# Performance work log

Hardware: AMD Instinct MI355X
Metric: run time of the kernel (lower is better)

The kernel has to match this reference:

```python
import jax, jax.numpy as jnp
import numpy as np

# (dv=3, dc=6)-regular Tanner graph: M checks, N=2M vars, E=M*dc edges
M, N, DV, DC, D, B, T = 1024, 2048, 3, 6, 8, 128, 5
CIN = DC * D          # check-MLP in/out dim = 48
VIN = DV * D + 1      # var-MLP in/out dim  = 25 (extra scalar = LLR)
HC, HV = 4 * CIN, 4 * VIN
EPS = 1e-6


def _graph():
    # variable j connects to checks (j + l) % M, l = 0..DV-1 -> every check has degree DC
    var_nbrs = (np.arange(N)[:, None] + np.arange(DV)[None, :]) % M   # [N, DV] check ids
    # var-edge id e = j*DV + l ; sort edges by check to get check-slot ordering
    order = np.argsort(var_nbrs.reshape(-1), kind='stable')           # check-edge p -> var-edge e
    chk_nbrs = (order // DV).reshape(M, DC)                           # var id in each check slot
    inv_order = np.argsort(order)                                     # var-edge e -> check-edge p
    return chk_nbrs, order, inv_order


def setup_inputs() -> dict:
    key = jax.random.key(0)
    ks = jax.random.split(key, 12)
    chk_nbrs, order, inv_order = _graph()
    prior = np.clip(np.random.default_rng(0).uniform(0.005, 0.05, size=N), EPS, 1 - EPS)
    prior_llr = jnp.asarray(np.log((1.0 - prior) / prior), jnp.float32)

    def lin_w(k, g, nin, nout):
        return jax.random.normal(k, (g, nin, nout), jnp.float32) / np.sqrt(nin)

    def lin_b(k, g, nout):
        return 0.02 * jax.random.normal(k, (g, nout), jnp.float32)

    return {
        "syndromes": jax.random.randint(ks[0], (B, M), 0, 2, jnp.int32),
        "prior_llr": prior_llr,
        "chk_w1": lin_w(ks[1], M, CIN, HC), "chk_b1": lin_b(ks[2], M, HC),
        "chk_w2": lin_w(ks[3], M, HC, CIN), "chk_b2": lin_b(ks[4], M, CIN),
        "var_w1": lin_w(ks[5], N, VIN, HV), "var_b1": lin_b(ks[6], N, HV),
        "var_w2": lin_w(ks[7], N, HV, VIN), "var_b2": lin_b(ks[8], N, VIN),
        "chk_nbrs": jnp.asarray(chk_nbrs, jnp.int32),      # [M, DC] var id per check slot
        "c2v_gather": jnp.asarray(inv_order, jnp.int32),   # var-edge -> check-edge perm
        "v2c_gather": jnp.asarray(order, jnp.int32),       # check-edge -> var-edge perm
    }


def reference(syndromes, prior_llr, chk_w1, chk_b1, chk_w2, chk_b2,
              var_w1, var_b1, var_w2, var_b2, chk_nbrs, c2v_gather, v2c_gather):
    synd_sgn = (1 - 2 * syndromes).astype(jnp.float32)                    # [B, M]
    prior_b = jnp.broadcast_to(prior_llr, (B, N))[..., None]              # [B, N, 1]

    def chk_mlp(x):  # x: [B, M, CIN], per-check grouped GEMM
        h = jax.nn.gelu(jnp.einsum('bmi,mih->bmh', x, chk_w1) + chk_b1, approximate=False)
        return jnp.einsum('bmh,mho->bmo', h, chk_w2) + chk_b2

    def var_mlp(x):  # x: [B, N, VIN]
        h = jax.nn.gelu(jnp.einsum('bni,nih->bnh', x, var_w1) + var_b1, approximate=False)
        return jnp.einsum('bnh,nho->bno', h, var_w2) + var_b2

    # init check in-messages: zeros with first component = prior LLR of neighbor var
    chk_in = jnp.zeros((B, M, DC, D), jnp.float32).at[..., 0].set(prior_llr[chk_nbrs][None])

    def step(chk_in, _):
        y = chk_mlp(chk_in.reshape(B, M, CIN)).reshape(B, M, DC, D)
        y = y * synd_sgn[:, :, None, None]                                # syndrome sign flip
        var_in = y.reshape(B, M * DC, D)[:, c2v_gather]                   # scatter c->v as gather
        x = jnp.concatenate([var_in.reshape(B, N, DV * D), prior_b], axis=-1)
        out = var_mlp(x)
        llr = out[..., DV * D]                                            # [B, N]
        msg = out[..., :DV * D].reshape(B, N * DV, D)
        chk_in_new = msg[:, v2c_gather].reshape(B, M, DC, D)              # scatter v->c as gather
        return chk_in_new, llr

    _, llrs = jax.lax.scan(step, chk_in, None, length=T)
    return llrs  # [T, B, N]
```

## Files before the change

kernel.cpp:

```cpp
#include <hip/hip_runtime.h>
#include <math.h>

#define MM 1024
#define NN 2048
#define BB 128
#define TT 5
#define EE 6144

typedef __bf16 bf16x8 __attribute__((ext_vector_type(8)));
typedef float  f32x4  __attribute__((ext_vector_type(4)));
typedef unsigned int u32x4 __attribute__((ext_vector_type(4)));
typedef unsigned int u32x2 __attribute__((ext_vector_type(2)));

__device__ __forceinline__ float gelu_fast(float x) {
    float xe = x * 0.70710678118654752f;
    float ax = fabsf(xe);
    float t  = __builtin_amdgcn_rcpf(1.0f + 0.3275911f * ax);
    float p  = t * (0.254829592f + t * (-0.284496736f + t * (1.421413741f +
               t * (-1.453152027f + t * 1.061405429f))));
    float er = 1.0f - p * __expf(-xe * xe);
    er = copysignf(er, xe);
    return 0.5f * x * (1.0f + er);
}

__device__ __forceinline__ void wave_lds_fence() {
    asm volatile("s_waitcnt lgkmcnt(0)" ::: "memory");
}

__global__ __launch_bounds__(256)
void init_kernel(const float* __restrict__ prior, __bf16* __restrict__ v2c)
{
    int idx = blockIdx.x * 256 + threadIdx.x;
    int e = idx >> 7;
    bf16x8 v;
    #pragma unroll
    for (int j = 0; j < 8; ++j) v[j] = (__bf16)0.0f;
    v[0] = (__bf16)prior[e / 3];
    *(bf16x8*)(v2c + (size_t)idx * 8) = v;
}

__global__ __launch_bounds__(256)
void prep_all(const float* __restrict__ cw1, const float* __restrict__ cw2,
              const float* __restrict__ vw1, const float* __restrict__ vw2,
              __bf16* __restrict__ wchk, __bf16* __restrict__ wvar)
{
    const int wid = blockIdx.x * 4 + (threadIdx.x >> 6);
    const int l = threadIdx.x & 63, qq = l >> 4, cc = l & 15;
    bf16x8 v;
    __bf16* dst;
    if (wid < MM * 42) {
        const int m = wid / 42, f = wid % 42;
        if (f < 24) {
            const int kt = f / 12, nt = f % 12;
            const float* s1 = cw1 + (size_t)m * (48 * 192);
            #pragma unroll
            for (int j = 0; j < 8; ++j) {
                int k = kt * 32 + qq * 8 + j;
                v[j] = (k < 48) ? (__bf16)s1[k * 192 + nt * 16 + cc] : (__bf16)0.0f;
            }
        } else {
            const int g = f - 24, kt = g / 3, nt = g % 3;
            const float* s2 = cw2 + (size_t)m * (192 * 48);
            #pragma unroll
            for (int j = 0; j < 8; ++j) {
                int k = kt * 32 + qq * 8 + j;
                v[j] = (__bf16)s2[k * 48 + nt * 16 + cc];
            }
        }
        dst = wchk + (size_t)m * 21504 + (f * 64 + l) * 8;
    } else {
        const int tsk = wid - MM * 42;
        const int nv = tsk / 15, f = tsk % 15;
        if (f < 7) {
            const float* s1 = vw1 + (size_t)nv * (25 * 100);
            #pragma unroll
            for (int j = 0; j < 8; ++j) {
                int k = qq * 8 + j, n = f * 16 + cc;
                v[j] = (k < 25 && n < 100) ? (__bf16)s1[k * 100 + n] : (__bf16)0.0f;
            }
        } else {
            const int g = f - 7, kt = g >> 1, nt = g & 1;
            const float* s2 = vw2 + (size_t)nv * (100 * 25);
            #pragma unroll
            for (int j = 0; j < 8; ++j) {
                int k = kt * 32 + qq * 8 + j, n = nt * 16 + cc;
                v[j] = (k < 100 && n < 25) ? (__bf16)s2[k * 25 + n] : (__bf16)0.0f;
            }
        }
        dst = wvar + (size_t)nv * 7680 + (f * 64 + l) * 8;
    }
    *(bf16x8*)dst = v;
}

__global__ __launch_bounds__(256, 4)
void chk_kernel(const __bf16* __restrict__ wchk,
                const float* __restrict__ b1g, const float* __restrict__ b2g,
                const int* __restrict__ syndromes,
                const int* __restrict__ v2c_gather,
                const __bf16* __restrict__ v2c, __bf16* __restrict__ c2v)
{
    const int m = blockIdx.x;
    const int tid = threadIdx.x;
    const int w = tid >> 6, l = tid & 63, q = l >> 4, c = l & 15;

    __shared__ __align__(16) __bf16 hb[4 * 3200];
    __bf16* myh = hb + w * 3200;

    const __bf16* wb = wchk + (size_t)m * 21504;

    float b1v[12], b2v[3], sg[8];
    #pragma unroll
    for (int nt = 0; nt < 12; ++nt) b1v[nt] = b1g[(size_t)m * 192 + nt * 16 + c];
    #pragma unroll
    for (int nt = 0; nt < 3; ++nt)  b2v[nt] = b2g[(size_t)m * 48 + nt * 16 + c];
    #pragma unroll
    for (int t2 = 0; t2 < 2; ++t2)
        #pragma unroll
        for (int r = 0; r < 4; ++r) {
            int row = t2 * 64 + w * 16 + q * 4 + r;
            sg[t2 * 4 + r] = (float)(1 - 2 * syndromes[(size_t)row * MM + m]);
        }

    const int e0 = v2c_gather[m * 6 + q];
    const int e1 = (q < 2) ? v2c_gather[m * 6 + 4 + q] : 0;

    for (int t2 = 0; t2 < 2; ++t2) {
        const int bt = t2 * 64 + w * 16;

        bf16x8 a0 = *(const bf16x8*)(v2c + ((size_t)e0 * BB + bt + c) * 8);
        bf16x8 a1;
        #pragma unroll
        for (int j = 0; j < 8; ++j) a1[j] = (__bf16)0.0f;
        if (q < 2) a1 = *(const bf16x8*)(v2c + ((size_t)e1 * BB + bt + c) * 8);

        f32x4 acc[12];
        #pragma unroll
        for (int nt = 0; nt < 12; ++nt) {
            bf16x8 bf0 = *(const bf16x8*)(wb + (nt * 64 + l) * 8);
            bf16x8 bf1 = *(const bf16x8*)(wb + ((12 + nt) * 64 + l) * 8);
            f32x4 z = {0.f, 0.f, 0.f, 0.f};
            z = __builtin_amdgcn_mfma_f32_16x16x32_bf16(a0, bf0, z, 0, 0, 0);
            z = __builtin_amdgcn_mfma_f32_16x16x32_bf16(a1, bf1, z, 0, 0, 0);
            acc[nt] = z;
        }

        #pragma unroll
        for (int nt = 0; nt < 12; ++nt) {
            #pragma unroll
            for (int r = 0; r < 4; ++r) {
                int row = q * 4 + r;
                myh[row * 200 + nt * 16 + c] = (__bf16)gelu_fast(acc[nt][r] + b1v[nt]);
            }
        }
        wave_lds_fence();

        f32x4 acc2[3];
        #pragma unroll
        for (int nt = 0; nt < 3; ++nt) acc2[nt] = (f32x4){0.f, 0.f, 0.f, 0.f};
        #pragma unroll
        for (int kt = 0; kt < 6; ++kt) {
            bf16x8 a = *(const bf16x8*)(myh + c * 200 + kt * 32 + q * 8);
            #pragma unroll
            for (int nt = 0; nt < 3; ++nt) {
                bf16x8 bfr = *(const bf16x8*)(wb + ((24 + kt * 3 + nt) * 64 + l) * 8);
                acc2[nt] = __builtin_amdgcn_mfma_f32_16x16x32_bf16(a, bfr, acc2[nt], 0, 0, 0);
            }
        }
        wave_lds_fence();

        #pragma unroll
        for (int nt = 0; nt < 3; ++nt) {
            #pragma unroll
            for (int r = 0; r < 4; ++r) {
                int row = q * 4 + r;
                myh[row * 72 + nt * 16 + c] = (__bf16)((acc2[nt][r] + b2v[nt]) * sg[t2 * 4 + r]);
            }
        }
        wave_lds_fence();

        {
            int s = l >> 4, row = l & 15;
            u32x4 vv = *(const u32x4*)(myh + row * 72 + s * 8);
            *(u32x4*)(c2v + ((size_t)(m * 6 + s) * BB + bt + row) * 8) = vv;
            if (l < 32) {
                int s2 = 4 + (l >> 4), row2 = l & 15;
                u32x4 v2 = *(const u32x4*)(myh + row2 * 72 + s2 * 8);
                *(u32x4*)(c2v + ((size_t)(m * 6 + s2) * BB + bt + row2) * 8) = v2;
            }
        }
        wave_lds_fence();
    }
}

__global__ __launch_bounds__(256, 4)
void var_kernel(const __bf16* __restrict__ wvar,
                const float* __restrict__ b1g, const float* __restrict__ b2g,
                const int* __restrict__ c2v_gather, const float* __restrict__ prior,
                const __bf16* __restrict__ c2v, __bf16* __restrict__ v2c,
                float* __restrict__ llr_out, int last)
{
    const int nv = blockIdx.x;
    const int tid = threadIdx.x;
    const int w = tid >> 6, l = tid & 63, q = l >> 4, c = l & 15;

    __shared__ __align__(16) __bf16 hb[4 * 2816];
    __bf16* myh = hb + w * 2816;
    __bf16* myy = myh + 2176;

    const __bf16* wb = wvar + (size_t)nv * 7680;

    {
        int r = l >> 2, g = l & 3;
        *(u32x2*)(myh + r * 136 + 112 + g * 4) = (u32x2){0, 0};
    }

    float b1v[7], b2v[2];
    #pragma unroll
    for (int nt = 0; nt < 7; ++nt) {
        int col = nt * 16 + c;
        b1v[nt] = (col < 100) ? b1g[(size_t)nv * 100 + col] : 0.0f;
    }
    #pragma unroll
    for (int nt = 0; nt < 2; ++nt) {
        int col = nt * 16 + c;
        b2v[nt] = (col < 25) ? b2g[(size_t)nv * 25 + col] : 0.0f;
    }
    const __bf16 prbf = (__bf16)prior[nv];
    const int ep = (q < 3) ? c2v_gather[nv * 3 + q] : 0;

    for (int t2 = 0; t2 < 2; ++t2) {
        const int bt = t2 * 64 + w * 16;

        bf16x8 a;
        #pragma unroll
        for (int j = 0; j < 8; ++j) a[j] = (__bf16)0.0f;
        if (q < 3) a = *(const bf16x8*)(c2v + ((size_t)ep * BB + bt + c) * 8);
        else       a[0] = prbf;

        f32x4 acc[7];
        #pragma unroll
        for (int nt = 0; nt < 7; ++nt) {
            bf16x8 bfr = *(const bf16x8*)(wb + (nt * 64 + l) * 8);
            f32x4 z = {0.f, 0.f, 0.f, 0.f};
            acc[nt] = __builtin_amdgcn_mfma_f32_16x16x32_bf16(a, bfr, z, 0, 0, 0);
        }

        #pragma unroll
        for (int nt = 0; nt < 7; ++nt) {
            #pragma unroll
            for (int r = 0; r < 4; ++r) {
                int row = q * 4 + r;
                myh[row * 136 + nt * 16 + c] = (__bf16)gelu_fast(acc[nt][r] + b1v[nt]);
            }
        }
        wave_lds_fence();

        f32x4 acc2[2];
        acc2[0] = (f32x4){0.f, 0.f, 0.f, 0.f};
        acc2[1] = (f32x4){0.f, 0.f, 0.f, 0.f};
        #pragma unroll
        for (int kt = 0; kt < 4; ++kt) {
            bf16x8 a2 = *(const bf16x8*)(myh + c * 136 + kt * 32 + q * 8);
            #pragma unroll
            for (int nt = 0; nt < 2; ++nt) {
                bf16x8 bfr = *(const bf16x8*)(wb + ((7 + kt * 2 + nt) * 64 + l) * 8);
                acc2[nt] = __builtin_amdgcn_mfma_f32_16x16x32_bf16(a2, bfr, acc2[nt], 0, 0, 0);
            }
        }
        wave_lds_fence();

        #pragma unroll
        for (int nt = 0; nt < 2; ++nt) {
            #pragma unroll
            for (int r = 0; r < 4; ++r) {
                int row = q * 4 + r, col = nt * 16 + c;
                float yv = acc2[nt][r] + b2v[nt];
                if (col < 24) myy[row * 40 + col] = (__bf16)yv;
                else if (col == 24) llr_out[(size_t)(bt + row) * NN + nv] = yv;
            }
        }
        wave_lds_fence();

        if (!last && l < 48) {
            int s = l >> 4, row = l & 15;
            u32x4 vv = *(const u32x4*)(myy + row * 40 + s * 8);
            *(u32x4*)(v2c + ((size_t)(nv * 3 + s) * BB + bt + row) * 8) = vv;
        }
        wave_lds_fence();
    }
}

extern "C" void kernel_launch(void* const* d_in, const int* in_sizes, int n_in,
                              void* d_out, int out_size, void* d_ws, size_t ws_size,
                              hipStream_t stream) {
    const int*   syndromes = (const int*)  d_in[0];
    const float* prior_llr = (const float*)d_in[1];
    const float* chk_w1    = (const float*)d_in[2];
    const float* chk_b1    = (const float*)d_in[3];
    const float* chk_w2    = (const float*)d_in[4];
    const float* chk_b2    = (const float*)d_in[5];
    const float* var_w1    = (const float*)d_in[6];
    const float* var_b1    = (const float*)d_in[7];
    const float* var_w2    = (const float*)d_in[8];
    const float* var_b2    = (const float*)d_in[9];
    const int*   c2v_g     = (const int*)  d_in[11];
    const int*   v2c_g     = (const int*)  d_in[12];

    float* out = (float*)d_out;

    __bf16* v2c  = (__bf16*)d_ws;
    __bf16* c2v  = v2c + (size_t)EE * BB * 8;
    __bf16* wchk = c2v + (size_t)EE * BB * 8;
    __bf16* wvar = wchk + (size_t)MM * 21504;

    prep_all<<<(MM * 42 + NN * 15) / 4, 256, 0, stream>>>(chk_w1, chk_w2,
                                                          var_w1, var_w2,
                                                          wchk, wvar);
    init_kernel<<<EE * BB / 256, 256, 0, stream>>>(prior_llr, v2c);

    for (int t = 0; t < TT; ++t) {
        chk_kernel<<<MM, 256, 0, stream>>>(wchk, chk_b1, chk_b2,
                                           syndromes, v2c_g, v2c, c2v);
        var_kernel<<<NN, 256, 0, stream>>>(wvar, var_b1, var_b2,
                                           c2v_g, prior_llr, c2v, v2c,
                                           out + (size_t)t * BB * NN,
                                           (t == TT - 1) ? 1 : 0);
    }
}
```

Before: 443.8 us.

## Stage per-node MLP weights in LDS and chunk check hidden layer

The check and variable kernels now copy each node's pre-packed bf16 weights into shared memory once per block, instead of having every wave read them from global memory on each batch half. The check kernel splits the hidden layer into three chunks of 64 columns that are fused into the second GEMM, which shrinks per-wave scratch space and register use. The prep kernel is reworked to issue unconditional clamped loads before masking, and the check kernel's occupancy hint drops to three blocks per CU to fit the larger LDS footprint. The trade-offs are an extra block-wide barrier plus lower occupancy, set against fewer redundant global and L2 weight reads.

```diff
diff --git a/kernel.cpp b/kernel.cpp
--- a/kernel.cpp
+++ b/kernel.cpp
@@ -46,6 +46,7 @@
 {
     const int wid = blockIdx.x * 4 + (threadIdx.x >> 6);
     const int l = threadIdx.x & 63, qq = l >> 4, cc = l & 15;
+    float tmp[8];
     bf16x8 v;
     __bf16* dst;
     if (wid < MM * 42) {
@@ -56,16 +57,21 @@
             #pragma unroll
             for (int j = 0; j < 8; ++j) {
                 int k = kt * 32 + qq * 8 + j;
-                v[j] = (k < 48) ? (__bf16)s1[k * 192 + nt * 16 + cc] : (__bf16)0.0f;
+                tmp[j] = s1[min(k, 47) * 192 + nt * 16 + cc];
+            }
+            #pragma unroll
+            for (int j = 0; j < 8; ++j) {
+                int k = kt * 32 + qq * 8 + j;
+                v[j] = (k < 48) ? (__bf16)tmp[j] : (__bf16)0.0f;
             }
         } else {
             const int g = f - 24, kt = g / 3, nt = g % 3;
             const float* s2 = cw2 + (size_t)m * (192 * 48);
             #pragma unroll
-            for (int j = 0; j < 8; ++j) {
-                int k = kt * 32 + qq * 8 + j;
-                v[j] = (__bf16)s2[k * 48 + nt * 16 + cc];
-            }
+            for (int j = 0; j < 8; ++j)
+                tmp[j] = s2[(kt * 32 + qq * 8 + j) * 48 + nt * 16 + cc];
+            #pragma unroll
+            for (int j = 0; j < 8; ++j) v[j] = (__bf16)tmp[j];
         }
         dst = wchk + (size_t)m * 21504 + (f * 64 + l) * 8;
     } else {
@@ -73,18 +79,30 @@
         const int nv = tsk / 15, f = tsk % 15;
         if (f < 7) {
             const float* s1 = vw1 + (size_t)nv * (25 * 100);
-            #pragma unroll
-            for (int j = 0; j < 8; ++j) {
-                int k = qq * 8 + j, n = f * 16 + cc;
-                v[j] = (k < 25 && n < 100) ? (__bf16)s1[k * 100 + n] : (__bf16)0.0f;
+            const int n = f * 16 + cc, nc = min(n, 99);
+            #pragma unroll
+            for (int j = 0; j < 8; ++j) {
+                int k = qq * 8 + j;
+                tmp[j] = s1[min(k, 24) * 100 + nc];
+            }
+            #pragma unroll
+            for (int j = 0; j < 8; ++j) {
+                int k = qq * 8 + j;
+                v[j] = (k < 25 && n < 100) ? (__bf16)tmp[j] : (__bf16)0.0f;
             }
         } else {
             const int g = f - 7, kt = g >> 1, nt = g & 1;
             const float* s2 = vw2 + (size_t)nv * (100 * 25);
-            #pragma unroll
-            for (int j = 0; j < 8; ++j) {
-                int k = kt * 32 + qq * 8 + j, n = nt * 16 + cc;
-                v[j] = (k < 100 && n < 25) ? (__bf16)s2[k * 25 + n] : (__bf16)0.0f;
+            const int n = nt * 16 + cc, nc = min(n, 24);
+            #pragma unroll
+            for (int j = 0; j < 8; ++j) {
+                int k = kt * 32 + qq * 8 + j;
+                tmp[j] = s2[min(k, 99) * 25 + nc];
+            }
+            #pragma unroll
+            for (int j = 0; j < 8; ++j) {
+                int k = kt * 32 + qq * 8 + j;
+                v[j] = (k < 100 && n < 25) ? (__bf16)tmp[j] : (__bf16)0.0f;
             }
         }
         dst = wvar + (size_t)nv * 7680 + (f * 64 + l) * 8;
@@ -92,7 +110,7 @@
     *(bf16x8*)dst = v;
 }
 
-__global__ __launch_bounds__(256, 4)
+__global__ __launch_bounds__(256, 3)
 void chk_kernel(const __bf16* __restrict__ wchk,
                 const float* __restrict__ b1g, const float* __restrict__ b2g,
                 const int* __restrict__ syndromes,
@@ -103,10 +121,14 @@
     const int tid = threadIdx.x;
     const int w = tid >> 6, l = tid & 63, q = l >> 4, c = l & 15;
 
-    __shared__ __align__(16) __bf16 hb[4 * 3200];
-    __bf16* myh = hb + w * 3200;
-
-    const __bf16* wb = wchk + (size_t)m * 21504;
+    __shared__ __align__(16) __bf16 wlds[21504];
+    __shared__ __align__(16) __bf16 scr[4 * 1152];
+
+    {
+        const __bf16* src = wchk + (size_t)m * 21504;
+        for (int i = tid; i < 2688; i += 256)
+            *(u32x4*)(wlds + i * 8) = *(const u32x4*)(src + i * 8);
+    }
 
     float b1v[12], b2v[3], sg[8];
     #pragma unroll
@@ -120,10 +142,13 @@
             int row = t2 * 64 + w * 16 + q * 4 + r;
             sg[t2 * 4 + r] = (float)(1 - 2 * syndromes[(size_t)row * MM + m]);
         }
-
     const int e0 = v2c_gather[m * 6 + q];
     const int e1 = (q < 2) ? v2c_gather[m * 6 + 4 + q] : 0;
 
+    __syncthreads();
+
+    __bf16* myc = scr + w * 1152;
+
     for (int t2 = 0; t2 < 2; ++t2) {
         const int bt = t2 * 64 + w * 16;
 
@@ -133,58 +158,64 @@
         for (int j = 0; j < 8; ++j) a1[j] = (__bf16)0.0f;
         if (q < 2) a1 = *(const bf16x8*)(v2c + ((size_t)e1 * BB + bt + c) * 8);
 
-        f32x4 acc[12];
-        #pragma unroll
-        for (int nt = 0; nt < 12; ++nt) {
-            bf16x8 bf0 = *(const bf16x8*)(wb + (nt * 64 + l) * 8);
-            bf16x8 bf1 = *(const bf16x8*)(wb + ((12 + nt) * 64 + l) * 8);
-            f32x4 z = {0.f, 0.f, 0.f, 0.f};
-            z = __builtin_amdgcn_mfma_f32_16x16x32_bf16(a0, bf0, z, 0, 0, 0);
-            z = __builtin_amdgcn_mfma_f32_16x16x32_bf16(a1, bf1, z, 0, 0, 0);
-            acc[nt] = z;
-        }
-
-        #pragma unroll
-        for (int nt = 0; nt < 12; ++nt) {
+        f32x4 acc2[3];
+        #pragma unroll
+        for (int nt = 0; nt < 3; ++nt) acc2[nt] = (f32x4){0.f, 0.f, 0.f, 0.f};
+
+        #pragma unroll
+        for (int ch = 0; ch < 3; ++ch) {
+            f32x4 acc[4];
+            #pragma unroll
+            for (int lnt = 0; lnt < 4; ++lnt) {
+                int nt = ch * 4 + lnt;
+                bf16x8 bf0 = *(const bf16x8*)(wlds + (nt * 64 + l) * 8);
+                bf16x8 bf1 = *(const bf16x8*)(wlds + ((12 + nt) * 64 + l) * 8);
+                f32x4 z = {0.f, 0.f, 0.f, 0.f};
+                z = __builtin_amdgcn_mfma_f32_16x16x32_bf16(a0, bf0, z, 0, 0, 0);
+                z = __builtin_amdgcn_mfma_f32_16x16x32_bf16(a1, bf1, z, 0, 0, 0);
+                acc[lnt] = z;
+            }
+            #pragma unroll
+            for (int lnt = 0; lnt < 4; ++lnt) {
+                #pragma unroll
+                for (int r = 0; r < 4; ++r) {
+                    int row = q * 4 + r;
+                    myc[row * 72 + lnt * 16 + c] =
+                        (__bf16)gelu_fast(acc[lnt][r] + b1v[ch * 4 + lnt]);
+                }
+            }
+            wave_lds_fence();
+            #pragma unroll
+            for (int ktl = 0; ktl < 2; ++ktl) {
+                bf16x8 aF = *(const bf16x8*)(myc + c * 72 + ktl * 32 + q * 8);
+                #pragma unroll
+                for (int nt = 0; nt < 3; ++nt) {
+                    bf16x8 bfr = *(const bf16x8*)(wlds +
+                        ((24 + (ch * 2 + ktl) * 3 + nt) * 64 + l) * 8);
+                    acc2[nt] = __builtin_amdgcn_mfma_f32_16x16x32_bf16(aF, bfr, acc2[nt], 0, 0, 0);
+                }
+            }
+            wave_lds_fence();
+        }
+
+        #pragma unroll
+        for (int nt = 0; nt < 3; ++nt) {
             #pragma unroll
             for (int r = 0; r < 4; ++r) {
                 int row = q * 4 + r;
-                myh[row * 200 + nt * 16 + c] = (__bf16)gelu_fast(acc[nt][r] + b1v[nt]);
-            }
-        }
-        wave_lds_fence();
-
-        f32x4 acc2[3];
-        #pragma unroll
-        for (int nt = 0; nt < 3; ++nt) acc2[nt] = (f32x4){0.f, 0.f, 0.f, 0.f};
-        #pragma unroll
-        for (int kt = 0; kt < 6; ++kt) {
-            bf16x8 a = *(const bf16x8*)(myh + c * 200 + kt * 32 + q * 8);
-            #pragma unroll
-            for (int nt = 0; nt < 3; ++nt) {
-                bf16x8 bfr = *(const bf16x8*)(wb + ((24 + kt * 3 + nt) * 64 + l) * 8);
-                acc2[nt] = __builtin_amdgcn_mfma_f32_16x16x32_bf16(a, bfr, acc2[nt], 0, 0, 0);
-            }
-        }
-        wave_lds_fence();
-
-        #pragma unroll
-        for (int nt = 0; nt < 3; ++nt) {
-            #pragma unroll
-            for (int r = 0; r < 4; ++r) {
-                int row = q * 4 + r;
-                myh[row * 72 + nt * 16 + c] = (__bf16)((acc2[nt][r] + b2v[nt]) * sg[t2 * 4 + r]);
+                myc[row * 56 + nt * 16 + c] =
+                    (__bf16)((acc2[nt][r] + b2v[nt]) * sg[t2 * 4 + r]);
             }
         }
         wave_lds_fence();
 
         {
             int s = l >> 4, row = l & 15;
-            u32x4 vv = *(const u32x4*)(myh + row * 72 + s * 8);
+            u32x4 vv = *(const u32x4*)(myc + row * 56 + s * 8);
             *(u32x4*)(c2v + ((size_t)(m * 6 + s) * BB + bt + row) * 8) = vv;
             if (l < 32) {
                 int s2 = 4 + (l >> 4), row2 = l & 15;
-                u32x4 v2 = *(const u32x4*)(myh + row2 * 72 + s2 * 8);
+                u32x4 v2 = *(const u32x4*)(myc + row2 * 56 + s2 * 8);
                 *(u32x4*)(c2v + ((size_t)(m * 6 + s2) * BB + bt + row2) * 8) = v2;
             }
         }
@@ -203,11 +234,17 @@
     const int tid = threadIdx.x;
     const int w = tid >> 6, l = tid & 63, q = l >> 4, c = l & 15;
 
+    __shared__ __align__(16) __bf16 wlds[7680];
     __shared__ __align__(16) __bf16 hb[4 * 2816];
+
+    {
+        const __bf16* src = wvar + (size_t)nv * 7680;
+        for (int i = tid; i < 960; i += 256)
+            *(u32x4*)(wlds + i * 8) = *(const u32x4*)(src + i * 8);
+    }
+
     __bf16* myh = hb + w * 2816;
     __bf16* myy = myh + 2176;
-
-    const __bf16* wb = wvar + (size_t)nv * 7680;
 
     {
         int r = l >> 2, g = l & 3;
@@ -228,6 +265,8 @@
     const __bf16 prbf = (__bf16)prior[nv];
     const int ep = (q < 3) ? c2v_gather[nv * 3 + q] : 0;
 
+    __syncthreads();
+
     for (int t2 = 0; t2 < 2; ++t2) {
         const int bt = t2 * 64 + w * 16;
 
@@ -240,7 +279,7 @@
         f32x4 acc[7];
         #pragma unroll
         for (int nt = 0; nt < 7; ++nt) {
-            bf16x8 bfr = *(const bf16x8*)(wb + (nt * 64 + l) * 8);
+            bf16x8 bfr = *(const bf16x8*)(wlds + (nt * 64 + l) * 8);
             f32x4 z = {0.f, 0.f, 0.f, 0.f};
             acc[nt] = __builtin_amdgcn_mfma_f32_16x16x32_bf16(a, bfr, z, 0, 0, 0);
         }
@@ -263,7 +302,7 @@
             bf16x8 a2 = *(const bf16x8*)(myh + c * 136 + kt * 32 + q * 8);
             #pragma unroll
             for (int nt = 0; nt < 2; ++nt) {
-                bf16x8 bfr = *(const bf16x8*)(wb + ((7 + kt * 2 + nt) * 64 + l) * 8);
+                bf16x8 bfr = *(const bf16x8*)(wlds + ((7 + kt * 2 + nt) * 64 + l) * 8);
                 acc2[nt] = __builtin_amdgcn_mfma_f32_16x16x32_bf16(a2, bfr, acc2[nt], 0, 0, 0);
             }
         }
```

After: 416.3 us. 6.2% less time.

## Use transposed MFMA layout, fold biases into weights, stage weights in LDS

Applied to the files above, without the earlier changes.

The MLPs are recomputed in transposed form (weights as the A operand, activations as B). The first layer's output fragments then feed the second layer's 16x16x16 MFMA directly from registers, which removes the LDS round-trip and wave fences for the hidden activations. Biases are folded into the weight matrices through an extra constant-one input row. Per-block weights are copied cooperatively into LDS, and outputs are packed and written straight to global memory. The cost is one block-wide sync per block, more LDS per block (chk occupancy hint lowered to 3), and a slightly larger prepacked weight buffer.

```diff
diff --git a/kernel.cpp b/kernel.cpp
--- a/kernel.cpp
+++ b/kernel.cpp
@@ -8,9 +8,16 @@
 #define EE 6144
 
 typedef __bf16 bf16x8 __attribute__((ext_vector_type(8)));
+typedef __bf16 bf16x4 __attribute__((ext_vector_type(4)));
+typedef short  s16x4  __attribute__((ext_vector_type(4)));
 typedef float  f32x4  __attribute__((ext_vector_type(4)));
 typedef unsigned int u32x4 __attribute__((ext_vector_type(4)));
 typedef unsigned int u32x2 __attribute__((ext_vector_type(2)));
+
+#define CHK_W_ELEMS 22272
+#define CHK_L2_OFF  12288
+#define VAR_W_ELEMS 7168
+#define VAR_L2_OFF  3584
 
 __device__ __forceinline__ float gelu_fast(float x) {
     float xe = x * 0.70710678118654752f;
@@ -23,8 +30,22 @@
     return 0.5f * x * (1.0f + er);
 }
 
-__device__ __forceinline__ void wave_lds_fence() {
-    asm volatile("s_waitcnt lgkmcnt(0)" ::: "memory");
+__device__ __forceinline__ f32x4 mfma16(bf16x4 a, bf16x4 b, f32x4 c) {
+#if __has_builtin(__builtin_amdgcn_mfma_f32_16x16x16bf16_1k)
+    return __builtin_amdgcn_mfma_f32_16x16x16bf16_1k(
+        __builtin_bit_cast(s16x4, a), __builtin_bit_cast(s16x4, b), c, 0, 0, 0);
+#else
+    f32x4 d;
+    asm volatile("v_mfma_f32_16x16x16_bf16 %0, %1, %2, %3\n\ts_nop 4"
+                 : "=v"(d) : "v"(a), "v"(b), "v"(c));
+    return d;
+#endif
+}
+
+__device__ __forceinline__ unsigned pack2(float a, float b) {
+    unsigned short ua = __builtin_bit_cast(unsigned short, (__bf16)a);
+    unsigned short ub = __builtin_bit_cast(unsigned short, (__bf16)b);
+    return (unsigned)ua | ((unsigned)ub << 16);
 }
 
 __global__ __launch_bounds__(256)
@@ -40,61 +61,109 @@
 }
 
 __global__ __launch_bounds__(256)
-void prep_all(const float* __restrict__ cw1, const float* __restrict__ cw2,
-              const float* __restrict__ vw1, const float* __restrict__ vw2,
+void prep_all(const float* __restrict__ cw1, const float* __restrict__ cb1,
+              const float* __restrict__ cw2, const float* __restrict__ cb2,
+              const float* __restrict__ vw1, const float* __restrict__ vb1,
+              const float* __restrict__ vw2, const float* __restrict__ vb2,
               __bf16* __restrict__ wchk, __bf16* __restrict__ wvar)
 {
     const int wid = blockIdx.x * 4 + (threadIdx.x >> 6);
-    const int l = threadIdx.x & 63, qq = l >> 4, cc = l & 15;
-    bf16x8 v;
-    __bf16* dst;
-    if (wid < MM * 42) {
-        const int m = wid / 42, f = wid % 42;
-        if (f < 24) {
-            const int kt = f / 12, nt = f % 12;
-            const float* s1 = cw1 + (size_t)m * (48 * 192);
-            #pragma unroll
-            for (int j = 0; j < 8; ++j) {
-                int k = kt * 32 + qq * 8 + j;
-                v[j] = (k < 48) ? (__bf16)s1[k * 192 + nt * 16 + cc] : (__bf16)0.0f;
+    const int l = threadIdx.x & 63, q = l >> 4, c = l & 15;
+
+    if (wid < 24576) {
+        const int m = wid / 24, f = wid % 24;
+        const int mt = f >> 1, kt = f & 1;
+        const int h = mt * 16 + c;
+        const float* s1 = cw1 + (size_t)m * (48 * 192);
+        float tmp[8];
+        #pragma unroll
+        for (int j = 0; j < 8; ++j) {
+            int k = kt * 32 + q * 8 + j;
+            tmp[j] = s1[min(k, 47) * 192 + h];
+        }
+        float bv = cb1[(size_t)m * 192 + h];
+        bf16x8 v;
+        #pragma unroll
+        for (int j = 0; j < 8; ++j) {
+            int k = kt * 32 + q * 8 + j;
+            float x = (k < 48) ? tmp[j] : ((k == 48) ? bv : 0.0f);
+            v[j] = (__bf16)x;
+        }
+        *(bf16x8*)(wchk + (size_t)m * CHK_W_ELEMS + f * 512 + l * 8) = v;
+    } else if (wid < 37888) {
+        const int t = wid - 24576;
+        const int m = t / 13, ks = t % 13;
+        __bf16* base = wchk + (size_t)m * CHK_W_ELEMS + CHK_L2_OFF;
+        if (ks < 12) {
+            const float* s2 = cw2 + (size_t)m * (192 * 48);
+            #pragma unroll
+            for (int mt = 0; mt < 3; ++mt) {
+                const int o = mt * 16 + c;
+                bf16x4 v;
+                #pragma unroll
+                for (int i = 0; i < 4; ++i)
+                    v[i] = (__bf16)s2[(ks * 16 + q * 4 + i) * 48 + o];
+                *(bf16x4*)(base + (ks * 3 + mt) * 256 + l * 4) = v;
             }
         } else {
-            const int g = f - 24, kt = g / 3, nt = g % 3;
-            const float* s2 = cw2 + (size_t)m * (192 * 48);
-            #pragma unroll
-            for (int j = 0; j < 8; ++j) {
-                int k = kt * 32 + qq * 8 + j;
-                v[j] = (__bf16)s2[k * 48 + nt * 16 + cc];
-            }
-        }
-        dst = wchk + (size_t)m * 21504 + (f * 64 + l) * 8;
+            #pragma unroll
+            for (int mt = 0; mt < 3; ++mt) {
+                const int o = mt * 16 + c;
+                float bv = cb2[(size_t)m * 48 + o];
+                bf16x4 v;
+                #pragma unroll
+                for (int i = 0; i < 4; ++i) v[i] = (__bf16)0.0f;
+                if (q == 0) v[0] = (__bf16)bv;
+                *(bf16x4*)(base + (12 * 3 + mt) * 256 + l * 4) = v;
+            }
+        }
+    } else if (wid < 52224) {
+        const int t = wid - 37888;
+        const int nv = t / 7, mt = t % 7;
+        const int h = mt * 16 + c, hc = min(h, 99);
+        const float* s1 = vw1 + (size_t)nv * (25 * 100);
+        float tmp[8];
+        #pragma unroll
+        for (int j = 0; j < 8; ++j)
+            tmp[j] = s1[min(q * 8 + j, 24) * 100 + hc];
+        float bv = vb1[(size_t)nv * 100 + hc];
+        bf16x8 v;
+        #pragma unroll
+        for (int j = 0; j < 8; ++j) {
+            int k = q * 8 + j;
+            float x = 0.0f;
+            if (h < 100) x = (k < 25) ? tmp[j] : ((k == 25) ? bv : 0.0f);
+            v[j] = (__bf16)x;
+        }
+        *(bf16x8*)(wvar + (size_t)nv * VAR_W_ELEMS + mt * 512 + l * 8) = v;
     } else {
-        const int tsk = wid - MM * 42;
-        const int nv = tsk / 15, f = tsk % 15;
-        if (f < 7) {
-            const float* s1 = vw1 + (size_t)nv * (25 * 100);
-            #pragma unroll
-            for (int j = 0; j < 8; ++j) {
-                int k = qq * 8 + j, n = f * 16 + cc;
-                v[j] = (k < 25 && n < 100) ? (__bf16)s1[k * 100 + n] : (__bf16)0.0f;
-            }
-        } else {
-            const int g = f - 7, kt = g >> 1, nt = g & 1;
-            const float* s2 = vw2 + (size_t)nv * (100 * 25);
-            #pragma unroll
-            for (int j = 0; j < 8; ++j) {
-                int k = kt * 32 + qq * 8 + j, n = nt * 16 + cc;
-                v[j] = (k < 100 && n < 25) ? (__bf16)s2[k * 25 + n] : (__bf16)0.0f;
-            }
-        }
-        dst = wvar + (size_t)nv * 7680 + (f * 64 + l) * 8;
-    }
-    *(bf16x8*)dst = v;
-}
-
-__global__ __launch_bounds__(256, 4)
+        const int t = wid - 52224;
+        const int nv = t / 7, ks = t % 7;
+        const float* s2 = vw2 + (size_t)nv * (100 * 25);
+        __bf16* base = wvar + (size_t)nv * VAR_W_ELEMS + VAR_L2_OFF;
+        #pragma unroll
+        for (int mt = 0; mt < 2; ++mt) {
+            const int o = mt * 16 + c, oc = min(o, 24);
+            float tmp[4];
+            #pragma unroll
+            for (int i = 0; i < 4; ++i)
+                tmp[i] = s2[min(ks * 16 + q * 4 + i, 99) * 25 + oc];
+            float bv = vb2[(size_t)nv * 25 + oc];
+            bf16x4 v;
+            #pragma unroll
+            for (int i = 0; i < 4; ++i) {
+                int k = ks * 16 + q * 4 + i;
+                float x = 0.0f;
+                if (o < 25) x = (k < 100) ? tmp[i] : ((k == 100) ? bv : 0.0f);
+                v[i] = (__bf16)x;
+            }
+            *(bf16x4*)(base + (ks * 2 + mt) * 256 + l * 4) = v;
+        }
+    }
+}
+
+__global__ __launch_bounds__(256, 3)
 void chk_kernel(const __bf16* __restrict__ wchk,
-                const float* __restrict__ b1g, const float* __restrict__ b2g,
                 const int* __restrict__ syndromes,
                 const int* __restrict__ v2c_gather,
                 const __bf16* __restrict__ v2c, __bf16* __restrict__ c2v)
@@ -103,98 +172,71 @@
     const int tid = threadIdx.x;
     const int w = tid >> 6, l = tid & 63, q = l >> 4, c = l & 15;
 
-    __shared__ __align__(16) __bf16 hb[4 * 3200];
-    __bf16* myh = hb + w * 3200;
-
-    const __bf16* wb = wchk + (size_t)m * 21504;
-
-    float b1v[12], b2v[3], sg[8];
-    #pragma unroll
-    for (int nt = 0; nt < 12; ++nt) b1v[nt] = b1g[(size_t)m * 192 + nt * 16 + c];
-    #pragma unroll
-    for (int nt = 0; nt < 3; ++nt)  b2v[nt] = b2g[(size_t)m * 48 + nt * 16 + c];
-    #pragma unroll
-    for (int t2 = 0; t2 < 2; ++t2)
-        #pragma unroll
-        for (int r = 0; r < 4; ++r) {
-            int row = t2 * 64 + w * 16 + q * 4 + r;
-            sg[t2 * 4 + r] = (float)(1 - 2 * syndromes[(size_t)row * MM + m]);
-        }
-
+    __shared__ __align__(16) __bf16 wlds[CHK_W_ELEMS];
+    {
+        const __bf16* src = wchk + (size_t)m * CHK_W_ELEMS;
+        for (int i = tid; i < CHK_W_ELEMS / 8; i += 256)
+            *(u32x4*)(wlds + i * 8) = *(const u32x4*)(src + i * 8);
+    }
     const int e0 = v2c_gather[m * 6 + q];
     const int e1 = (q < 2) ? v2c_gather[m * 6 + 4 + q] : 0;
+    __syncthreads();
 
     for (int t2 = 0; t2 < 2; ++t2) {
         const int bt = t2 * 64 + w * 16;
 
-        bf16x8 a0 = *(const bf16x8*)(v2c + ((size_t)e0 * BB + bt + c) * 8);
-        bf16x8 a1;
-        #pragma unroll
-        for (int j = 0; j < 8; ++j) a1[j] = (__bf16)0.0f;
-        if (q < 2) a1 = *(const bf16x8*)(v2c + ((size_t)e1 * BB + bt + c) * 8);
+        bf16x8 b0 = *(const bf16x8*)(v2c + ((size_t)e0 * BB + bt + c) * 8);
+        bf16x8 b1f;
+        #pragma unroll
+        for (int j = 0; j < 8; ++j) b1f[j] = (__bf16)0.0f;
+        if (q < 2)       b1f = *(const bf16x8*)(v2c + ((size_t)e1 * BB + bt + c) * 8);
+        else if (q == 2) b1f[0] = (__bf16)1.0f;
 
         f32x4 acc[12];
         #pragma unroll
-        for (int nt = 0; nt < 12; ++nt) {
-            bf16x8 bf0 = *(const bf16x8*)(wb + (nt * 64 + l) * 8);
-            bf16x8 bf1 = *(const bf16x8*)(wb + ((12 + nt) * 64 + l) * 8);
+        for (int mt = 0; mt < 12; ++mt) {
+            bf16x8 a0 = *(const bf16x8*)(wlds + (mt * 2 + 0) * 512 + l * 8);
+            bf16x8 a1 = *(const bf16x8*)(wlds + (mt * 2 + 1) * 512 + l * 8);
             f32x4 z = {0.f, 0.f, 0.f, 0.f};
-            z = __builtin_amdgcn_mfma_f32_16x16x32_bf16(a0, bf0, z, 0, 0, 0);
-            z = __builtin_amdgcn_mfma_f32_16x16x32_bf16(a1, bf1, z, 0, 0, 0);
-            acc[nt] = z;
-        }
-
-        #pragma unroll
-        for (int nt = 0; nt < 12; ++nt) {
-            #pragma unroll
-            for (int r = 0; r < 4; ++r) {
-                int row = q * 4 + r;
-                myh[row * 200 + nt * 16 + c] = (__bf16)gelu_fast(acc[nt][r] + b1v[nt]);
-            }
-        }
-        wave_lds_fence();
+            z = __builtin_amdgcn_mfma_f32_16x16x32_bf16(a0, b0, z, 0, 0, 0);
+            z = __builtin_amdgcn_mfma_f32_16x16x32_bf16(a1, b1f, z, 0, 0, 0);
+            acc[mt] = z;
+        }
 
         f32x4 acc2[3];
         #pragma unroll
-        for (int nt = 0; nt < 3; ++nt) acc2[nt] = (f32x4){0.f, 0.f, 0.f, 0.f};
-        #pragma unroll
-        for (int kt = 0; kt < 6; ++kt) {
-            bf16x8 a = *(const bf16x8*)(myh + c * 200 + kt * 32 + q * 8);
-            #pragma unroll
-            for (int nt = 0; nt < 3; ++nt) {
-                bf16x8 bfr = *(const bf16x8*)(wb + ((24 + kt * 3 + nt) * 64 + l) * 8);
-                acc2[nt] = __builtin_amdgcn_mfma_f32_16x16x32_bf16(a, bfr, acc2[nt], 0, 0, 0);
-            }
-        }
-        wave_lds_fence();
-
-        #pragma unroll
-        for (int nt = 0; nt < 3; ++nt) {
-            #pragma unroll
-            for (int r = 0; r < 4; ++r) {
-                int row = q * 4 + r;
-                myh[row * 72 + nt * 16 + c] = (__bf16)((acc2[nt][r] + b2v[nt]) * sg[t2 * 4 + r]);
-            }
-        }
-        wave_lds_fence();
-
-        {
-            int s = l >> 4, row = l & 15;
-            u32x4 vv = *(const u32x4*)(myh + row * 72 + s * 8);
-            *(u32x4*)(c2v + ((size_t)(m * 6 + s) * BB + bt + row) * 8) = vv;
-            if (l < 32) {
-                int s2 = 4 + (l >> 4), row2 = l & 15;
-                u32x4 v2 = *(const u32x4*)(myh + row2 * 72 + s2 * 8);
-                *(u32x4*)(c2v + ((size_t)(m * 6 + s2) * BB + bt + row2) * 8) = v2;
-            }
-        }
-        wave_lds_fence();
+        for (int mt = 0; mt < 3; ++mt) acc2[mt] = (f32x4){0.f, 0.f, 0.f, 0.f};
+        #pragma unroll
+        for (int ks = 0; ks < 13; ++ks) {
+            bf16x4 bf;
+            if (ks < 12) {
+                #pragma unroll
+                for (int r = 0; r < 4; ++r) bf[r] = (__bf16)gelu_fast(acc[ks][r]);
+            } else {
+                #pragma unroll
+                for (int r = 0; r < 4; ++r) bf[r] = (__bf16)0.0f;
+                if (q == 0) bf[0] = (__bf16)1.0f;
+            }
+            #pragma unroll
+            for (int mt = 0; mt < 3; ++mt) {
+                bf16x4 af = *(const bf16x4*)(wlds + CHK_L2_OFF + (ks * 3 + mt) * 256 + l * 4);
+                acc2[mt] = mfma16(af, bf, acc2[mt]);
+            }
+        }
+
+        const float sg = (float)(1 - 2 * syndromes[(size_t)(bt + c) * MM + m]);
+        #pragma unroll
+        for (int mt = 0; mt < 3; ++mt) {
+            u32x2 pv = { pack2(acc2[mt][0] * sg, acc2[mt][1] * sg),
+                         pack2(acc2[mt][2] * sg, acc2[mt][3] * sg) };
+            int s = 2 * mt + (q >> 1);
+            *(u32x2*)(c2v + ((size_t)(m * 6 + s) * BB + bt + c) * 8 + (q & 1) * 4) = pv;
+        }
     }
 }
 
 __global__ __launch_bounds__(256, 4)
 void var_kernel(const __bf16* __restrict__ wvar,
-                const float* __restrict__ b1g, const float* __restrict__ b2g,
                 const int* __restrict__ c2v_gather, const float* __restrict__ prior,
                 const __bf16* __restrict__ c2v, __bf16* __restrict__ v2c,
                 float* __restrict__ llr_out, int last)
@@ -203,90 +245,59 @@
     const int tid = threadIdx.x;
     const int w = tid >> 6, l = tid & 63, q = l >> 4, c = l & 15;
 
-    __shared__ __align__(16) __bf16 hb[4 * 2816];
-    __bf16* myh = hb + w * 2816;
-    __bf16* myy = myh + 2176;
-
-    const __bf16* wb = wvar + (size_t)nv * 7680;
-
+    __shared__ __align__(16) __bf16 wlds[VAR_W_ELEMS];
     {
-        int r = l >> 2, g = l & 3;
-        *(u32x2*)(myh + r * 136 + 112 + g * 4) = (u32x2){0, 0};
-    }
-
-    float b1v[7], b2v[2];
-    #pragma unroll
-    for (int nt = 0; nt < 7; ++nt) {
-        int col = nt * 16 + c;
-        b1v[nt] = (col < 100) ? b1g[(size_t)nv * 100 + col] : 0.0f;
-    }
-    #pragma unroll
-    for (int nt = 0; nt < 2; ++nt) {
-        int col = nt * 16 + c;
-        b2v[nt] = (col < 25) ? b2g[(size_t)nv * 25 + col] : 0.0f;
-    }
+        const __bf16* src = wvar + (size_t)nv * VAR_W_ELEMS;
+        for (int i = tid; i < VAR_W_ELEMS / 8; i += 256)
+            *(u32x4*)(wlds + i * 8) = *(const u32x4*)(src + i * 8);
+    }
+    const int ep = (q < 3) ? c2v_gather[nv * 3 + q] : 0;
     const __bf16 prbf = (__bf16)prior[nv];
-    const int ep = (q < 3) ? c2v_gather[nv * 3 + q] : 0;
+    __syncthreads();
 
     for (int t2 = 0; t2 < 2; ++t2) {
         const int bt = t2 * 64 + w * 16;
 
-        bf16x8 a;
-        #pragma unroll
-        for (int j = 0; j < 8; ++j) a[j] = (__bf16)0.0f;
-        if (q < 3) a = *(const bf16x8*)(c2v + ((size_t)ep * BB + bt + c) * 8);
-        else       a[0] = prbf;
+        bf16x8 b0;
+        #pragma unroll
+        for (int j = 0; j < 8; ++j) b0[j] = (__bf16)0.0f;
+        if (q < 3) b0 = *(const bf16x8*)(c2v + ((size_t)ep * BB + bt + c) * 8);
+        else { b0[0] = prbf; b0[1] = (__bf16)1.0f; }
 
         f32x4 acc[7];
         #pragma unroll
-        for (int nt = 0; nt < 7; ++nt) {
-            bf16x8 bfr = *(const bf16x8*)(wb + (nt * 64 + l) * 8);
+        for (int mt = 0; mt < 7; ++mt) {
+            bf16x8 a0 = *(const bf16x8*)(wlds + mt * 512 + l * 8);
             f32x4 z = {0.f, 0.f, 0.f, 0.f};
-            acc[nt] = __builtin_amdgcn_mfma_f32_16x16x32_bf16(a, bfr, z, 0, 0, 0);
-        }
-
-        #pragma unroll
-        for (int nt = 0; nt < 7; ++nt) {
-            #pragma unroll
-            for (int r = 0; r < 4; ++r) {
-                int row = q * 4 + r;
-                myh[row * 136 + nt * 16 + c] = (__bf16)gelu_fast(acc[nt][r] + b1v[nt]);
-            }
-        }
-        wave_lds_fence();
+            acc[mt] = __builtin_amdgcn_mfma_f32_16x16x32_bf16(a0, b0, z, 0, 0, 0);
+        }
 
         f32x4 acc2[2];
         acc2[0] = (f32x4){0.f, 0.f, 0.f, 0.f};
         acc2[1] = (f32x4){0.f, 0.f, 0.f, 0.f};
         #pragma unroll
-        for (int kt = 0; kt < 4; ++kt) {
-            bf16x8 a2 = *(const bf16x8*)(myh + c * 136 + kt * 32 + q * 8);
-            #pragma unroll
-            for (int nt = 0; nt < 2; ++nt) {
-                bf16x8 bfr = *(const bf16x8*)(wb + ((7 + kt * 2 + nt) * 64 + l) * 8);
-                acc2[nt] = __builtin_amdgcn_mfma_f32_16x16x32_bf16(a2, bfr, acc2[nt], 0, 0, 0);
-            }
-        }
-        wave_lds_fence();
-
-        #pragma unroll
-        for (int nt = 0; nt < 2; ++nt) {
-            #pragma unroll
-            for (int r = 0; r < 4; ++r) {
-                int row = q * 4 + r, col = nt * 16 + c;
-                float yv = acc2[nt][r] + b2v[nt];
-                if (col < 24) myy[row * 40 + col] = (__bf16)yv;
-                else if (col == 24) llr_out[(size_t)(bt + row) * NN + nv] = yv;
-            }
-        }
-        wave_lds_fence();
-
-        if (!last && l < 48) {
-            int s = l >> 4, row = l & 15;
-            u32x4 vv = *(const u32x4*)(myy + row * 40 + s * 8);
-            *(u32x4*)(v2c + ((size_t)(nv * 3 + s) * BB + bt + row) * 8) = vv;
-        }
-        wave_lds_fence();
+        for (int ks = 0; ks < 7; ++ks) {
+            bf16x4 bf;
+            #pragma unroll
+            for (int r = 0; r < 4; ++r) bf[r] = (__bf16)gelu_fast(acc[ks][r]);
+            if (ks == 6 && q == 1) bf[0] = (__bf16)1.0f;
+            #pragma unroll
+            for (int mt = 0; mt < 2; ++mt) {
+                bf16x4 af = *(const bf16x4*)(wlds + VAR_L2_OFF + (ks * 2 + mt) * 256 + l * 4);
+                acc2[mt] = mfma16(af, bf, acc2[mt]);
+            }
+        }
+
+        if (!last) {
+            u32x2 p0 = { pack2(acc2[0][0], acc2[0][1]), pack2(acc2[0][2], acc2[0][3]) };
+            int s0 = q >> 1;
+            *(u32x2*)(v2c + ((size_t)(nv * 3 + s0) * BB + bt + c) * 8 + (q & 1) * 4) = p0;
+            if (q < 2) {
+                u32x2 p1 = { pack2(acc2[1][0], acc2[1][1]), pack2(acc2[1][2], acc2[1][3]) };
+                *(u32x2*)(v2c + ((size_t)(nv * 3 + 2) * BB + bt + c) * 8 + (q & 1) * 4) = p1;
+            }
+        }
+        if (q == 2) llr_out[(size_t)(bt + c) * NN + nv] = acc2[1][0];
     }
 }
 
@@ -311,18 +322,16 @@
     __bf16* v2c  = (__bf16*)d_ws;
     __bf16* c2v  = v2c + (size_t)EE * BB * 8;
     __bf16* wchk = c2v + (size_t)EE * BB * 8;
-    __bf16* wvar = wchk + (size_t)MM * 21504;
-
-    prep_all<<<(MM * 42 + NN * 15) / 4, 256, 0, stream>>>(chk_w1, chk_w2,
-                                                          var_w1, var_w2,
-                                                          wchk, wvar);
+    __bf16* wvar = wchk + (size_t)MM * CHK_W_ELEMS;
+
+    prep_all<<<16640, 256, 0, stream>>>(chk_w1, chk_b1, chk_w2, chk_b2,
+                                        var_w1, var_b1, var_w2, var_b2,
+                                        wchk, wvar);
     init_kernel<<<EE * BB / 256, 256, 0, stream>>>(prior_llr, v2c);
 
     for (int t = 0; t < TT; ++t) {
-        chk_kernel<<<MM, 256, 0, stream>>>(wchk, chk_b1, chk_b2,
-                                           syndromes, v2c_g, v2c, c2v);
-        var_kernel<<<NN, 256, 0, stream>>>(wvar, var_b1, var_b2,
-                                           c2v_g, prior_llr, c2v, v2c,
+        chk_kernel<<<MM, 256, 0, stream>>>(wchk, syndromes, v2c_g, v2c, c2v);
+        var_kernel<<<NN, 256, 0, stream>>>(wvar, c2v_g, prior_llr, c2v, v2c,
                                            out + (size_t)t * BB * NN,
                                            (t == TT - 1) ? 1 : 0);
     }
```

Measured after the change: 565.4 us. 27.4% more time.
